# Kernel optimization log

Hardware: AMD Instinct MI355X
Metric: run time of the kernel (lower is better)

The kernel has to match this reference:

```python
import jax, jax.numpy as jnp
import numpy as np

BS, L, D, H, BLOCKS = 2, 8192, 1024, 16, 16
BC = L // BLOCKS          # block_ctx = 512
HD = D // H               # head dim = 64
SCALE2 = 1.0 / float(np.sqrt(HD))  # (scale*scale) with scale = HD**-0.25


def setup_inputs() -> dict:
    key = jax.random.key(0)
    k0, k1, k2 = jax.random.split(key, 3)
    return {
        "x": jax.random.normal(k0, (BS, L, D), jnp.float32),
        "w_attn": jax.random.normal(k1, (D, 3 * D), jnp.float32) * 0.02,
        "b_attn": jnp.zeros((3 * D,), jnp.float32),
        "w_proj": jax.random.normal(k2, (D, D), jnp.float32) * 0.02,
        "b_proj": jnp.zeros((D,), jnp.float32),
    }


def _block_attn(q, k, v):
    # q, k, v: [BS, L, D]; block-local causal attention (attn_func=1, eval path)
    nb = BS * BLOCKS
    def heads(x):
        # [BS, L, D] -> [nb, BC, D] -> [nb, H, BC, HD]
        return x.reshape(nb, BC, H, HD).transpose(0, 2, 1, 3)
    qh, kh, vh = heads(q), heads(k), heads(v)
    w = jnp.einsum('bhqd,bhkd->bhqk', qh, kh) * SCALE2          # [nb, H, BC, BC]
    w = w.astype(jnp.float32)
    mask = jnp.tril(jnp.ones((BC, BC), jnp.float32))
    w = w * mask + (-1e9) * (1.0 - mask)
    w = jax.nn.softmax(w, axis=-1)
    a = jnp.einsum('bhqk,bhkd->bhqd', w, vh)                    # [nb, H, BC, HD]
    return a.transpose(0, 2, 1, 3).reshape(BS, L, D)


def reference(x, w_attn, b_attn, w_proj, b_proj):
    qkv = x @ w_attn + b_attn                                   # Conv1D c_attn
    q, k, v = jnp.split(qkv, 3, axis=-1)
    a = _block_attn(q, k, v)
    return a @ w_proj + b_proj                                  # Conv1D c_proj
```

## Files before the change

kernel.cpp:

```cpp
#include <hip/hip_runtime.h>
#include <stdint.h>


typedef __bf16 bf16x8 __attribute__((ext_vector_type(8)));
typedef short short8 __attribute__((ext_vector_type(8)));
typedef float f32x4 __attribute__((ext_vector_type(4)));
typedef unsigned short ushort4v __attribute__((ext_vector_type(4)));
typedef unsigned short ushort8v __attribute__((ext_vector_type(8)));

#define GLOAD_LDS16(g, l)                                                      \
  __builtin_amdgcn_global_load_lds(                                            \
      (const __attribute__((address_space(1))) void*)(g),                      \
      (__attribute__((address_space(3))) void*)(l), 16, 0, 0)

static __device__ __forceinline__ f32x4 mfma16(short8 a, short8 b, f32x4 c) {
  return __builtin_amdgcn_mfma_f32_16x16x32_bf16(
      __builtin_bit_cast(bf16x8, a), __builtin_bit_cast(bf16x8, b), c, 0, 0, 0);
}

static __device__ __forceinline__ unsigned short f2bf(float f) {
  unsigned u = __builtin_bit_cast(unsigned, f);
  u += 0x7FFFu + ((u >> 16) & 1u);
  return (unsigned short)(u >> 16);
}

__global__ __launch_bounds__(256) void convert_bf16(
    const float* __restrict__ in, unsigned short* __restrict__ out, int n8) {
  for (int i = blockIdx.x * 256 + threadIdx.x; i < n8; i += gridDim.x * 256) {
    f32x4 lo = *(const f32x4*)(in + (size_t)i * 8);
    f32x4 hi = *(const f32x4*)(in + (size_t)i * 8 + 4);
    ushort8v v;
    v[0] = f2bf(lo[0]); v[1] = f2bf(lo[1]); v[2] = f2bf(lo[2]); v[3] = f2bf(lo[3]);
    v[4] = f2bf(hi[0]); v[5] = f2bf(hi[1]); v[6] = f2bf(hi[2]); v[7] = f2bf(hi[3]);
    *(ushort8v*)(out + (size_t)i * 8) = v;
  }
}

__global__ __launch_bounds__(256) void transposeW(
    const float* __restrict__ in, unsigned short* __restrict__ out,
    int K, int N) {
  __shared__ float tile[64][68];
  int tn = blockIdx.x * 64, tk = blockIdx.y * 64;
  int tid = threadIdx.x;
#pragma unroll
  for (int i = 0; i < 4; ++i) {
    int ch = i * 256 + tid;
    int r = ch >> 4, c4 = (ch & 15) << 2;
    f32x4 v = *(const f32x4*)(in + (size_t)(tk + r) * N + tn + c4);
    tile[r][c4] = v[0]; tile[r][c4 + 1] = v[1];
    tile[r][c4 + 2] = v[2]; tile[r][c4 + 3] = v[3];
  }
  __syncthreads();
#pragma unroll
  for (int i = 0; i < 4; ++i) {
    int ch = i * 256 + tid;
    int r = ch >> 4, c4 = (ch & 15) << 2;
    ushort4v v;
    v[0] = f2bf(tile[c4][r]);     v[1] = f2bf(tile[c4 + 1][r]);
    v[2] = f2bf(tile[c4 + 2][r]); v[3] = f2bf(tile[c4 + 3][r]);
    *(ushort4v*)(out + (size_t)(tn + r) * K + tk + c4) = v;
  }
}

template <bool C_F32>
__global__ __launch_bounds__(256) void gemm_bt(
    const unsigned short* __restrict__ A, int lda,
    const unsigned short* __restrict__ Bt, int ldb,
    const float* __restrict__ bias,
    void* __restrict__ Cptr, int ldc,
    int Ntiles, int K) {
  __shared__ unsigned short sA[128 * 64];
  __shared__ unsigned short sB[128 * 64];
  int bid = blockIdx.x;
  int nwg = gridDim.x;
  int swz = (bid & 7) * (nwg >> 3) + (bid >> 3);
  int bm = swz / Ntiles, bn = swz % Ntiles;
  int tid = threadIdx.x;
  int lane = tid & 63, wave = tid >> 6;
  int wr = wave >> 1, wc = wave & 1;
  int g = lane >> 4, cx = lane & 15;

  const unsigned short* srcA[4];
  const unsigned short* srcB[4];
  unsigned short* dstA[4];
  unsigned short* dstB[4];
#pragma unroll
  for (int i = 0; i < 4; ++i) {
    int c = i * 256 + tid;
    int r = c >> 3, pc = c & 7;
    int cc = pc ^ (r & 7);
    srcA[i] = A + (size_t)(bm * 128 + r) * lda + cc * 8;
    srcB[i] = Bt + (size_t)(bn * 128 + r) * ldb + cc * 8;
    dstA[i] = sA + (i * 256 + wave * 64) * 8;
    dstB[i] = sB + (i * 256 + wave * 64) * 8;
  }

  f32x4 zero4 = {0.f, 0.f, 0.f, 0.f};
  f32x4 acc[4][4];
#pragma unroll
  for (int a = 0; a < 4; ++a)
#pragma unroll
    for (int b = 0; b < 4; ++b) acc[a][b] = zero4;

  for (int kt = 0; kt < K; kt += 64) {
#pragma unroll
    for (int i = 0; i < 4; ++i) {
      GLOAD_LDS16(srcA[i] + kt, dstA[i]);
      GLOAD_LDS16(srcB[i] + kt, dstB[i]);
    }
    __syncthreads();
#pragma unroll
    for (int ks = 0; ks < 2; ++ks) {
      short8 af[4], bfr[4];
#pragma unroll
      for (int mi = 0; mi < 4; ++mi) {
        int row = wr * 64 + mi * 16 + cx;
        unsigned off = (unsigned)(row * 128 + ks * 64 + g * 16);
        off ^= (unsigned)((row & 7) << 4);
        af[mi] = *(const short8*)((const char*)sA + off);
      }
#pragma unroll
      for (int ni = 0; ni < 4; ++ni) {
        int row = wc * 64 + ni * 16 + cx;
        unsigned off = (unsigned)(row * 128 + ks * 64 + g * 16);
        off ^= (unsigned)((row & 7) << 4);
        bfr[ni] = *(const short8*)((const char*)sB + off);
      }
#pragma unroll
      for (int mi = 0; mi < 4; ++mi)
#pragma unroll
        for (int ni = 0; ni < 4; ++ni)
          acc[mi][ni] = mfma16(af[mi], bfr[ni], acc[mi][ni]);
    }
    __syncthreads();
  }

  float bv[4];
#pragma unroll
  for (int ni = 0; ni < 4; ++ni)
    bv[ni] = bias[bn * 128 + wc * 64 + ni * 16 + cx];

#pragma unroll
  for (int mi = 0; mi < 4; ++mi)
#pragma unroll
    for (int ni = 0; ni < 4; ++ni) {
      int col = bn * 128 + wc * 64 + ni * 16 + cx;
#pragma unroll
      for (int ri = 0; ri < 4; ++ri) {
        int row = bm * 128 + wr * 64 + mi * 16 + g * 4 + ri;
        float v = acc[mi][ni][ri] + bv[ni];
        if (C_F32)
          ((float*)Cptr)[(size_t)row * ldc + col] = v;
        else
          ((unsigned short*)Cptr)[(size_t)row * ldc + col] = f2bf(v);
      }
    }
}

__global__ __launch_bounds__(256) void attn_block(unsigned short* __restrict__ qkv) {
  const int LDQ = 3072;
  int bid = blockIdx.x;
  int pair = bid & 1;
  int nbh = bid >> 1;
  int nb = nbh >> 4, h = nbh & 15;
  int rowblk = nb << 9;
  int tid = threadIdx.x, lane = tid & 63, wave = tid >> 6;
  int g = lane >> 4, cx = lane & 15;

  __shared__ unsigned short sK[64 * 64];
  __shared__ unsigned short sVT[64 * 64];
  __shared__ unsigned short sP[4][32 * 64];
  unsigned short* myP = sP[wave];

  const unsigned short* srcK[2];
  const unsigned short* srcV[2];
  unsigned short* dstK[2];
  int kr_[2], d8_[2];
#pragma unroll
  for (int i = 0; i < 2; ++i) {
    int c = i * 256 + tid;
    int r = c >> 3, pc = c & 7, cc = pc ^ (r & 7);
    srcK[i] = qkv + (size_t)(rowblk + r) * LDQ + 1024 + h * 64 + cc * 8;
    srcV[i] = qkv + (size_t)(rowblk + r) * LDQ + 2048 + h * 64 + pc * 8;
    dstK[i] = sK + (i * 256 + wave * 64) * 8;
    kr_[i] = r; d8_[i] = pc;
  }

  f32x4 zero4 = {0.f, 0.f, 0.f, 0.f};
  const float CEXP = 0.125f * 1.44269504088896f;

  for (int qq = 0; qq < 2; ++qq) {
    int qs = qq ? (pair ? 2 : 3) : (pair ? 1 : 0);
    int ntiles = 2 * qs + 2;
    int qb0 = qs * 128 + wave * 16;

    short8 qreg[2][2];
#pragma unroll
    for (int ni = 0; ni < 2; ++ni) {
      int qrow = rowblk + qb0 + ni * 64 + cx;
      const unsigned short* qp = qkv + (size_t)qrow * LDQ + h * 64 + g * 8;
      qreg[ni][0] = *(const short8*)qp;
      qreg[ni][1] = *(const short8*)(qp + 32);
    }

    f32x4 ot[2][4];
#pragma unroll
    for (int a = 0; a < 2; ++a)
#pragma unroll
      for (int b = 0; b < 4; ++b) ot[a][b] = zero4;
    float m_run[2] = {-1e30f, -1e30f};
    float l_run[2] = {0.f, 0.f};

    for (int t = 0; t < ntiles; ++t) {
      size_t tadv = (size_t)(t * 64) * LDQ;
      short8 vv0 = *(const short8*)(srcV[0] + tadv);
      short8 vv1 = *(const short8*)(srcV[1] + tadv);
      GLOAD_LDS16(srcK[0] + tadv, dstK[0]);
      GLOAD_LDS16(srcK[1] + tadv, dstK[1]);
#pragma unroll
      for (int j = 0; j < 8; ++j) {
        int d0 = d8_[0] * 8 + j, d1 = d8_[1] * 8 + j;
        unsigned o0 = (unsigned)(d0 * 128 + kr_[0] * 2) ^
                      (unsigned)((((d8_[0] ^ j) & 7)) << 4);
        unsigned o1 = (unsigned)(d1 * 128 + kr_[1] * 2) ^
                      (unsigned)((((d8_[1] ^ j) & 7)) << 4);
        *(unsigned short*)((char*)sVT + o0) = (unsigned short)vv0[j];
        *(unsigned short*)((char*)sVT + o1) = (unsigned short)vv1[j];
      }
      __syncthreads();

      bool live0 = (t * 64) <= (qb0 + 15);

      f32x4 s[4][2];
#pragma unroll
      for (int a = 0; a < 4; ++a)
#pragma unroll
        for (int b = 0; b < 2; ++b) s[a][b] = zero4;
#pragma unroll
      for (int ks = 0; ks < 2; ++ks) {
        short8 kf[4];
#pragma unroll
        for (int mi = 0; mi < 4; ++mi) {
          int row = mi * 16 + cx;
          unsigned off = (unsigned)(row * 128 + ks * 64 + g * 16);
          off ^= (unsigned)((row & 7) << 4);
          kf[mi] = *(const short8*)((const char*)sK + off);
        }
        if (live0) {
#pragma unroll
          for (int mi = 0; mi < 4; ++mi)
            s[mi][0] = mfma16(kf[mi], qreg[0][ks], s[mi][0]);
        }
#pragma unroll
        for (int mi = 0; mi < 4; ++mi)
          s[mi][1] = mfma16(kf[mi], qreg[1][ks], s[mi][1]);
      }

      float rescv[2] = {1.f, 1.f};
#pragma unroll
      for (int ni = 0; ni < 2; ++ni) {
        if (ni == 0 && !live0) continue;
        int qbase = qb0 + ni * 64;
        int qloc = qbase + cx;
        if ((t * 64 + 63) > qbase) {
#pragma unroll
          for (int mi = 0; mi < 4; ++mi)
#pragma unroll
            for (int ri = 0; ri < 4; ++ri) {
              int kk = t * 64 + mi * 16 + g * 4 + ri;
              if (kk > qloc) s[mi][ni][ri] = -3e38f;
            }
        }
        float tm = -3e38f;
#pragma unroll
        for (int mi = 0; mi < 4; ++mi)
          tm = fmaxf(tm, fmaxf(fmaxf(s[mi][ni][0], s[mi][ni][1]),
                               fmaxf(s[mi][ni][2], s[mi][ni][3])));
        tm = fmaxf(tm, __shfl_xor(tm, 16));
        tm = fmaxf(tm, __shfl_xor(tm, 32));
        float mnew = fmaxf(m_run[ni], tm);
        float resc = exp2f((m_run[ni] - mnew) * CEXP);
        float tsum = 0.f;
#pragma unroll
        for (int mi = 0; mi < 4; ++mi)
#pragma unroll
          for (int ri = 0; ri < 4; ++ri) {
            float p = exp2f((s[mi][ni][ri] - mnew) * CEXP);
            s[mi][ni][ri] = p;
            tsum += p;
          }
        tsum += __shfl_xor(tsum, 16);
        tsum += __shfl_xor(tsum, 32);
        l_run[ni] = l_run[ni] * resc + tsum;
        m_run[ni] = mnew;
        rescv[ni] = resc;
      }

#pragma unroll
      for (int ni = 0; ni < 2; ++ni) {
        if (ni == 0 && !live0) continue;
#pragma unroll
        for (int nd = 0; nd < 4; ++nd) {
          ot[ni][nd][0] *= rescv[ni]; ot[ni][nd][1] *= rescv[ni];
          ot[ni][nd][2] *= rescv[ni]; ot[ni][nd][3] *= rescv[ni];
        }
#pragma unroll
        for (int mi = 0; mi < 4; ++mi) {
          ushort4v pk;
          pk[0] = f2bf(s[mi][ni][0]); pk[1] = f2bf(s[mi][ni][1]);
          pk[2] = f2bf(s[mi][ni][2]); pk[3] = f2bf(s[mi][ni][3]);
          int row = ni * 16 + cx;
          unsigned off = (unsigned)(row * 128 + mi * 32 + g * 8);
          off ^= (unsigned)((row & 7) << 4);
          *(ushort4v*)((char*)myP + off) = pk;
        }
      }

#pragma unroll
      for (int ks = 0; ks < 2; ++ks) {
        short8 vf[4];
#pragma unroll
        for (int nd = 0; nd < 4; ++nd) {
          int d = nd * 16 + cx;
          unsigned off = (unsigned)(d * 128 + ks * 64 + g * 16);
          off ^= (unsigned)((((d >> 3) ^ d) & 7) << 4);
          vf[nd] = *(const short8*)((const char*)sVT + off);
        }
#pragma unroll
        for (int mq = 0; mq < 2; ++mq) {
          if (mq == 0 && !live0) continue;
          int row = mq * 16 + cx;
          unsigned off = (unsigned)(row * 128 + ks * 64 + g * 16);
          off ^= (unsigned)((row & 7) << 4);
          short8 pb = *(const short8*)((const char*)myP + off);
#pragma unroll
          for (int nd = 0; nd < 4; ++nd)
            ot[mq][nd] = mfma16(vf[nd], pb, ot[mq][nd]);
        }
      }
      __syncthreads();
    }

#pragma unroll
    for (int mq = 0; mq < 2; ++mq) {
      float linv = 1.0f / fmaxf(l_run[mq], 1e-30f);
      int qrow = rowblk + qb0 + mq * 64 + cx;
#pragma unroll
      for (int nd = 0; nd < 4; ++nd) {
        ushort4v w4;
        w4[0] = f2bf(ot[mq][nd][0] * linv); w4[1] = f2bf(ot[mq][nd][1] * linv);
        w4[2] = f2bf(ot[mq][nd][2] * linv); w4[3] = f2bf(ot[mq][nd][3] * linv);
        int col = h * 64 + nd * 16 + g * 4;
        *(ushort4v*)(qkv + (size_t)qrow * LDQ + col) = w4;
      }
    }
  }
}

extern "C" void kernel_launch(void* const* d_in, const int* in_sizes, int n_in,
                              void* d_out, int out_size, void* d_ws, size_t ws_size,
                              hipStream_t stream) {
  const float* x      = (const float*)d_in[0];
  const float* w_attn = (const float*)d_in[1];
  const float* b_attn = (const float*)d_in[2];
  const float* w_proj = (const float*)d_in[3];
  const float* b_proj = (const float*)d_in[4];
  float* out = (float*)d_out;

  char* ws = (char*)d_ws;
  unsigned short* qkv = (unsigned short*)ws;
  unsigned short* wAT = (unsigned short*)(ws + (size_t)16384 * 3072 * 2);
  unsigned short* wPT = wAT + (size_t)3072 * 1024;
  unsigned short* xbf = (unsigned short*)d_out;

  transposeW<<<dim3(48, 16), 256, 0, stream>>>(w_attn, wAT, 1024, 3072);
  transposeW<<<dim3(16, 16), 256, 0, stream>>>(w_proj, wPT, 1024, 1024);
  convert_bf16<<<2048, 256, 0, stream>>>(x, xbf, 16384 * 1024 / 8);

  gemm_bt<false><<<128 * 24, 256, 0, stream>>>(
      xbf, 1024, wAT, 1024, b_attn, (void*)qkv, 3072, 24, 1024);

  attn_block<<<1024, 256, 0, stream>>>(qkv);

  gemm_bt<true><<<128 * 8, 256, 0, stream>>>(
      qkv, 3072, wPT, 1024, b_proj, (void*)out, 1024, 8, 1024);
}
```

Measured before the change: 284.9 us.

## Enlarge GEMM tiles to 256x256 with 8 waves and double-buffered LDS prefetch

Replaces the 128x128, 4-wave GEMM with a 256x256, 512-thread kernel used for both the QKV and output projections. Each wave now computes a 128x64 sub-tile. The next K-tile is loaded into a second LDS buffer while the current one is consumed, using explicit vmcnt waits and raw barriers, and MFMA priority is raised during compute. The goal is more operand reuse per global load and less load-latency stall between K steps. The cost is 128KB of LDS and more accumulator registers, which limits occupancy to one block per CU. The output-projection GEMM also launches only 256 workgroups.

```diff
diff --git a/kernel.cpp b/kernel.cpp
--- a/kernel.cpp
+++ b/kernel.cpp
@@ -63,91 +63,121 @@
 }
 
 template <bool C_F32>
-__global__ __launch_bounds__(256) void gemm_bt(
+__global__ __launch_bounds__(512, 2) void gemm256(
     const unsigned short* __restrict__ A, int lda,
     const unsigned short* __restrict__ Bt, int ldb,
     const float* __restrict__ bias,
     void* __restrict__ Cptr, int ldc,
     int Ntiles, int K) {
-  __shared__ unsigned short sA[128 * 64];
-  __shared__ unsigned short sB[128 * 64];
+  __shared__ unsigned short sA[2][256 * 64];
+  __shared__ unsigned short sB[2][256 * 64];
   int bid = blockIdx.x;
   int nwg = gridDim.x;
   int swz = (bid & 7) * (nwg >> 3) + (bid >> 3);
   int bm = swz / Ntiles, bn = swz % Ntiles;
   int tid = threadIdx.x;
   int lane = tid & 63, wave = tid >> 6;
-  int wr = wave >> 1, wc = wave & 1;
+  int wr = wave >> 2, wc = wave & 3;
   int g = lane >> 4, cx = lane & 15;
 
   const unsigned short* srcA[4];
   const unsigned short* srcB[4];
-  unsigned short* dstA[4];
-  unsigned short* dstB[4];
+  int dstoff[4];
 #pragma unroll
   for (int i = 0; i < 4; ++i) {
-    int c = i * 256 + tid;
+    int c = i * 512 + tid;
     int r = c >> 3, pc = c & 7;
     int cc = pc ^ (r & 7);
-    srcA[i] = A + (size_t)(bm * 128 + r) * lda + cc * 8;
-    srcB[i] = Bt + (size_t)(bn * 128 + r) * ldb + cc * 8;
-    dstA[i] = sA + (i * 256 + wave * 64) * 8;
-    dstB[i] = sB + (i * 256 + wave * 64) * 8;
+    srcA[i] = A + (size_t)(bm * 256 + r) * lda + cc * 8;
+    srcB[i] = Bt + (size_t)(bn * 256 + r) * ldb + cc * 8;
+    dstoff[i] = (i * 512 + wave * 64) * 8;
   }
 
   f32x4 zero4 = {0.f, 0.f, 0.f, 0.f};
-  f32x4 acc[4][4];
-#pragma unroll
-  for (int a = 0; a < 4; ++a)
+  f32x4 acc[8][4];
+#pragma unroll
+  for (int a = 0; a < 8; ++a)
 #pragma unroll
     for (int b = 0; b < 4; ++b) acc[a][b] = zero4;
 
-  for (int kt = 0; kt < K; kt += 64) {
-#pragma unroll
-    for (int i = 0; i < 4; ++i) {
-      GLOAD_LDS16(srcA[i] + kt, dstA[i]);
-      GLOAD_LDS16(srcB[i] + kt, dstB[i]);
-    }
-    __syncthreads();
-#pragma unroll
-    for (int ks = 0; ks < 2; ++ks) {
-      short8 af[4], bfr[4];
-#pragma unroll
-      for (int mi = 0; mi < 4; ++mi) {
-        int row = wr * 64 + mi * 16 + cx;
-        unsigned off = (unsigned)(row * 128 + ks * 64 + g * 16);
-        off ^= (unsigned)((row & 7) << 4);
-        af[mi] = *(const short8*)((const char*)sA + off);
-      }
-#pragma unroll
-      for (int ni = 0; ni < 4; ++ni) {
+  int NT = K >> 6;
+
+#pragma unroll
+  for (int i = 0; i < 4; ++i) {
+    GLOAD_LDS16(srcA[i], sA[0] + dstoff[i]);
+    GLOAD_LDS16(srcB[i], sB[0] + dstoff[i]);
+  }
+
+  for (int t = 0; t < NT; ++t) {
+    int p = t & 1;
+    if (t + 1 < NT) {
+      int kt = (t + 1) * 64;
+#pragma unroll
+      for (int i = 0; i < 4; ++i) {
+        GLOAD_LDS16(srcA[i] + kt, sA[p ^ 1] + dstoff[i]);
+        GLOAD_LDS16(srcB[i] + kt, sB[p ^ 1] + dstoff[i]);
+      }
+      asm volatile("s_waitcnt vmcnt(8)" ::: "memory");
+    } else {
+      asm volatile("s_waitcnt vmcnt(0)" ::: "memory");
+    }
+    __builtin_amdgcn_sched_barrier(0);
+    __builtin_amdgcn_s_barrier();
+    __builtin_amdgcn_sched_barrier(0);
+
+    const char* bA = (const char*)sA[p];
+    const char* bB = (const char*)sB[p];
+    short8 bfr[4][2];
+#pragma unroll
+    for (int ni = 0; ni < 4; ++ni)
+#pragma unroll
+      for (int ks = 0; ks < 2; ++ks) {
         int row = wc * 64 + ni * 16 + cx;
-        unsigned off = (unsigned)(row * 128 + ks * 64 + g * 16);
-        off ^= (unsigned)((row & 7) << 4);
-        bfr[ni] = *(const short8*)((const char*)sB + off);
-      }
-#pragma unroll
-      for (int mi = 0; mi < 4; ++mi)
+        unsigned off = (unsigned)(row * 128 + ks * 64 + g * 16) ^
+                       ((unsigned)(row & 7) << 4);
+        bfr[ni][ks] = *(const short8*)(bB + off);
+      }
+#pragma unroll
+    for (int q = 0; q < 4; ++q) {
+      short8 af[2][2];
+#pragma unroll
+      for (int mm = 0; mm < 2; ++mm)
+#pragma unroll
+        for (int ks = 0; ks < 2; ++ks) {
+          int row = wr * 128 + (q * 2 + mm) * 16 + cx;
+          unsigned off = (unsigned)(row * 128 + ks * 64 + g * 16) ^
+                         ((unsigned)(row & 7) << 4);
+          af[mm][ks] = *(const short8*)(bA + off);
+        }
+      __builtin_amdgcn_s_setprio(1);
+#pragma unroll
+      for (int mm = 0; mm < 2; ++mm)
 #pragma unroll
         for (int ni = 0; ni < 4; ++ni)
-          acc[mi][ni] = mfma16(af[mi], bfr[ni], acc[mi][ni]);
-    }
-    __syncthreads();
+#pragma unroll
+          for (int ks = 0; ks < 2; ++ks)
+            acc[q * 2 + mm][ni] = mfma16(af[mm][ks], bfr[ni][ks],
+                                         acc[q * 2 + mm][ni]);
+      __builtin_amdgcn_s_setprio(0);
+    }
+    __builtin_amdgcn_sched_barrier(0);
+    __builtin_amdgcn_s_barrier();
+    __builtin_amdgcn_sched_barrier(0);
   }
 
   float bv[4];
 #pragma unroll
   for (int ni = 0; ni < 4; ++ni)
-    bv[ni] = bias[bn * 128 + wc * 64 + ni * 16 + cx];
-
-#pragma unroll
-  for (int mi = 0; mi < 4; ++mi)
+    bv[ni] = bias[bn * 256 + wc * 64 + ni * 16 + cx];
+
+#pragma unroll
+  for (int mi = 0; mi < 8; ++mi)
 #pragma unroll
     for (int ni = 0; ni < 4; ++ni) {
-      int col = bn * 128 + wc * 64 + ni * 16 + cx;
+      int col = bn * 256 + wc * 64 + ni * 16 + cx;
 #pragma unroll
       for (int ri = 0; ri < 4; ++ri) {
-        int row = bm * 128 + wr * 64 + mi * 16 + g * 4 + ri;
+        int row = bm * 256 + wr * 128 + mi * 16 + g * 4 + ri;
         float v = acc[mi][ni][ri] + bv[ni];
         if (C_F32)
           ((float*)Cptr)[(size_t)row * ldc + col] = v;
@@ -377,11 +407,11 @@
   transposeW<<<dim3(16, 16), 256, 0, stream>>>(w_proj, wPT, 1024, 1024);
   convert_bf16<<<2048, 256, 0, stream>>>(x, xbf, 16384 * 1024 / 8);
 
-  gemm_bt<false><<<128 * 24, 256, 0, stream>>>(
-      xbf, 1024, wAT, 1024, b_attn, (void*)qkv, 3072, 24, 1024);
+  gemm256<false><<<768, 512, 0, stream>>>(
+      xbf, 1024, wAT, 1024, b_attn, (void*)qkv, 3072, 12, 1024);
 
   attn_block<<<1024, 256, 0, stream>>>(qkv);
 
-  gemm_bt<true><<<128 * 8, 256, 0, stream>>>(
-      qkv, 3072, wPT, 1024, b_proj, (void*)out, 1024, 8, 1024);
-}
+  gemm256<true><<<256, 512, 0, stream>>>(
+      qkv, 3072, wPT, 1024, b_proj, (void*)out, 1024, 4, 1024);
+}
```

After: 255.8 us. 10.2% less time.
